# Optimization experiments

Measured on AMD Instinct MI355X. Metric: run time of the kernel, lower is better.

Reference implementation:

```python
import jax, jax.numpy as jnp
import numpy as np

B, D = 65536, 256      # batch, state dim (= hidden_dims[0])
H1, H2 = 256, 256      # hidden_dims
N_STEPS = 40           # fixed RK4 steps over t in [0, 1]
BN_EPS = 1e-3          # keras BatchNormalization default epsilon


def setup_inputs() -> dict:
    key = jax.random.key(0)
    ks = jax.random.split(key, 8)
    s = 0.05  # small init keeps dynamics smooth/stable
    return {
        "y0": jax.random.normal(ks[0], (B, D), dtype=jnp.float32),
        "W1": jax.random.normal(ks[1], (D, H1), dtype=jnp.float32) * s,
        "b1": jnp.zeros((H1,), jnp.float32),
        "g1": jnp.ones((H1,), jnp.float32),
        "be1": jnp.zeros((H1,), jnp.float32),
        "m1": jnp.zeros((H1,), jnp.float32),
        "v1": jnp.ones((H1,), jnp.float32),
        "W2": jax.random.normal(ks[2], (H1, H2), dtype=jnp.float32) * s,
        "b2": jnp.zeros((H2,), jnp.float32),
        "g2": jnp.ones((H2,), jnp.float32),
        "be2": jnp.zeros((H2,), jnp.float32),
        "m2": jnp.zeros((H2,), jnp.float32),
        "v2": jnp.ones((H2,), jnp.float32),
        "Wo": jax.random.normal(ks[3], (H2, D), dtype=jnp.float32) * s,
        "bo": jnp.zeros((D,), jnp.float32),
    }


def _ode_func(y, W1, b1, g1, be1, m1, v1, W2, b2, g2, be2, m2, v2, Wo, bo):
    # Dense(relu) -> BatchNorm(inference, moving stats) -> Dropout(inactive), x2, then Dense(tanh)
    h = jax.nn.relu(y @ W1 + b1)
    h = g1 * (h - m1) * jax.lax.rsqrt(v1 + BN_EPS) + be1
    h = jax.nn.relu(h @ W2 + b2)
    h = g2 * (h - m2) * jax.lax.rsqrt(v2 + BN_EPS) + be2
    return jnp.tanh(h @ Wo + bo)


def reference(y0, W1, b1, g1, be1, m1, v1, W2, b2, g2, be2, m2, v2, Wo, bo):
    # Integrate dy/dt = f(y) (autonomous) from t=0 to t=1 with fixed-step RK4.
    # (The original uses tfp adaptive BDF; RK4 is the clean deterministic stand-in
    # for the same continuous-time solution.)
    dt = jnp.float32(1.0 / N_STEPS)
    f = lambda y: _ode_func(y, W1, b1, g1, be1, m1, v1, W2, b2, g2, be2, m2, v2, Wo, bo)

    def step(y, _):
        k1 = f(y)
        k2 = f(y + 0.5 * dt * k1)
        k3 = f(y + 0.5 * dt * k2)
        k4 = f(y + dt * k3)
        return y + (dt / 6.0) * (k1 + 2.0 * k2 + 2.0 * k3 + k4), None

    y_final, _ = jax.lax.scan(step, y0, None, length=N_STEPS)
    return y_final
```

## Files before the change

### kernel.cpp

```cpp
#include <hip/hip_runtime.h>
#include <hip/hip_fp16.h>


typedef unsigned short u16;
typedef unsigned int   u32;
typedef __attribute__((ext_vector_type(8))) short bf16x8;
typedef __attribute__((ext_vector_type(4))) float f32x4;

#define BN_EPS 1e-3f
#define NROWS  65536
#define BM     128
#define NTHR   512
#define WT_ELEMS 196608
#define LDS_BIAS 131072
#define LDS_SIZE (131072 + 3072)

__device__ __forceinline__ u16 f2bf(float f) {
    u32 u = __float_as_uint(f);
    u32 r = u + 0x7FFFu + ((u >> 16) & 1u);
    return (u16)(r >> 16);
}
__device__ __forceinline__ float bf2f(u16 h) {
    return __uint_as_float(((u32)h) << 16);
}
__device__ __forceinline__ float fast_tanh(float x) {
    float e = __expf(2.0f * x);
    return 1.0f - __fdividef(2.0f, e + 1.0f);
}
__device__ __forceinline__ u32 pack_h2(float a, float b) {
    __half2 h = __floats2half2_rn(a, b);
    return *reinterpret_cast<u32*>(&h);
}
__device__ __forceinline__ float2 unpack_h2(u32 v) {
    __half2 h = *reinterpret_cast<__half2*>(&v);
    return __half22float2(h);
}
__device__ __forceinline__ u32 pack_bf2(float a, float b) {
    return ((u32)f2bf(b) << 16) | (u32)f2bf(a);
}
__device__ __forceinline__ float2 unpack_bf2(u32 p) {
    return make_float2(__uint_as_float(p << 16),
                       __uint_as_float(p & 0xFFFF0000u));
}

#define SWZ(row, kb) (((row) << 10) + ((kb) ^ (((row) & 7) << 4)))

__global__ void prep_bias(const float* __restrict__ b2,
                          const float* __restrict__ g1, const float* __restrict__ be1,
                          const float* __restrict__ m1, const float* __restrict__ v1,
                          const float* __restrict__ W2,
                          const float* __restrict__ bo,
                          const float* __restrict__ g2, const float* __restrict__ be2,
                          const float* __restrict__ m2, const float* __restrict__ v2,
                          const float* __restrict__ Wo,
                          float* __restrict__ b2o, float* __restrict__ boo) {
    int t = threadIdx.x;
    if (t < 256) {
        float s = b2[t];
        for (int i = 0; i < 256; ++i) {
            float s1 = g1[i] * rsqrtf(v1[i] + BN_EPS);
            float t1 = be1[i] - s1 * m1[i];
            s += t1 * W2[i * 256 + t];
        }
        b2o[t] = s;
    } else {
        int j = t - 256;
        float s = bo[j];
        for (int i = 0; i < 256; ++i) {
            float s2 = g2[i] * rsqrtf(v2[i] + BN_EPS);
            float t2 = be2[i] - s2 * m2[i];
            s += t2 * Wo[i * 256 + j];
        }
        boo[j] = s;
    }
}

__global__ void prep_weights(const float* __restrict__ W1, const float* __restrict__ W2,
                             const float* __restrict__ Wo,
                             const float* __restrict__ g1, const float* __restrict__ v1,
                             const float* __restrict__ g2, const float* __restrict__ v2,
                             u16* __restrict__ Wt) {
    int tid = blockIdx.x * 256 + threadIdx.x;
    if (tid >= 3 * 768 * 256) return;
    int l   = tid / (768 * 256);
    int r   = tid % (768 * 256);
    int kp  = r >> 8;
    int col = r & 255;
    int ok  = kp & 255;
    float w;
    if (l == 0)      w = W1[ok * 256 + col];
    else if (l == 1) w = W2[ok * 256 + col] * (g1[ok] * rsqrtf(v1[ok] + BN_EPS));
    else             w = Wo[ok * 256 + col] * (g2[ok] * rsqrtf(v2[ok] + BN_EPS));
    u16 hi = f2bf(w);
    u16 out = (kp < 512) ? hi : f2bf(w - bf2f(hi));
    int ks = kp >> 5, gg = (kp >> 3) & 3, j = kp & 7, cb = col >> 4, cc = col & 15;
    Wt[(size_t)l * WT_ELEMS + ks * 8192 + cb * 512 + cc * 32 + gg * 8 + j] = out;
}

__global__ __launch_bounds__(NTHR)
__attribute__((amdgpu_waves_per_eu(2, 2)))
void ode_persistent(const float* __restrict__ y0, float* __restrict__ yout,
                    const u16* __restrict__ Wt,
                    const float* __restrict__ b1, const float* __restrict__ b2o,
                    const float* __restrict__ boo) {
    extern __shared__ char smem[];
    float* bias_lds = reinterpret_cast<float*>(smem + LDS_BIAS);
    const int t = threadIdx.x;
    const size_t rowbase = (size_t)blockIdx.x * BM;
    const int lane = t & 63, wid = t >> 6;
    const int wr = wid >> 2, wc = wid & 3;
    const int c16 = lane & 15, g = lane >> 4;

    for (int i = t; i < 768; i += NTHR) {
        float v = (i < 256) ? b1[i] : ((i < 512) ? b2o[i - 256] : boo[i - 512]);
        bias_lds[i] = v;
    }

    f32x4 Y[4][4];
    u32   Kp[4][4][2];
    u32   A2[4][4][2];

#pragma unroll
    for (int m = 0; m < 4; ++m)
#pragma unroll
        for (int n = 0; n < 4; ++n) {
            const int col = wc * 64 + n * 16 + c16;
#pragma unroll
            for (int j = 0; j < 4; ++j) {
                const int row = wr * 64 + m * 16 + g * 4 + j;
                Y[m][n][j] = y0[(rowbase + row) * 256 + col];
            }
            Kp[m][n][0] = 0u; Kp[m][n][1] = 0u;
            A2[m][n][0] = 0u; A2[m][n][1] = 0u;
        }
    __syncthreads();

    const float dt  = 1.0f / 40.0f;
    const float c2  = 0.5f * dt;
    const float w16 = dt / 6.0f, w13 = dt / 3.0f;

    for (int it = 0; it < 160; ++it) {
        const int stage = it & 3;
        const float c = (stage == 0) ? 0.0f : ((stage == 3) ? dt : c2);
        const float w = (stage == 1 || stage == 2) ? w13 : w16;

#pragma unroll
        for (int m = 0; m < 4; ++m)
#pragma unroll
            for (int n = 0; n < 4; ++n) {
                const int col2 = (wc * 64 + n * 16 + c16) * 2;
                const float2 k01 = unpack_bf2(Kp[m][n][0]);
                const float2 k23 = unpack_bf2(Kp[m][n][1]);
                const float kj[4] = {k01.x, k01.y, k23.x, k23.y};
#pragma unroll
                for (int j = 0; j < 4; ++j) {
                    const int row = wr * 64 + m * 16 + g * 4 + j;
                    const float x = fmaf(c, kj[j], Y[m][n][j]);
                    const u32 xb = __float_as_uint(x);
                    const u16 hi = (u16)(xb >> 16);
                    const float fl = x - __uint_as_float(xb & 0xFFFF0000u);
                    *reinterpret_cast<u16*>(smem + SWZ(row, col2))       = hi;
                    *reinterpret_cast<u16*>(smem + SWZ(row, 512 + col2)) = f2bf(fl);
                }
            }
        __syncthreads();

        f32x4 ACC[4][4];

#pragma unroll 1
        for (int l = 0; l < 3; ++l) {
            const u16* __restrict__ wt = Wt + (size_t)l * WT_ELEMS;

#pragma unroll
            for (int n = 0; n < 4; ++n) {
                const float bv = bias_lds[l * 256 + wc * 64 + n * 16 + c16];
                const f32x4 b4 = {bv, bv, bv, bv};
#pragma unroll
                for (int m = 0; m < 4; ++m) ACC[m][n] = b4;
            }

#pragma unroll 2
            for (int ks = 0; ks < 24; ++ks) {
                const int kfull = ks * 32;
                const int kloc  = (kfull >= 512) ? (kfull - 512) : kfull;
                const int kb    = kloc * 2 + g * 16;
                bf16x8 av[4], bv[4];
#pragma unroll
                for (int m = 0; m < 4; ++m) {
                    const int row = wr * 64 + m * 16 + c16;
                    av[m] = *reinterpret_cast<const bf16x8*>(smem + SWZ(row, kb));
                }
                const u16* wp = wt + (size_t)(ks * 16 + wc * 4) * 512 + c16 * 32 + g * 8;
#pragma unroll
                for (int n = 0; n < 4; ++n)
                    bv[n] = *reinterpret_cast<const bf16x8*>(wp + n * 512);
#pragma unroll
                for (int m = 0; m < 4; ++m)
#pragma unroll
                    for (int n = 0; n < 4; ++n)
                        ACC[m][n] = __builtin_amdgcn_mfma_f32_16x16x32_bf16(
                            av[m], bv[n], ACC[m][n], 0, 0, 0);
            }
            __syncthreads();

            if (l < 2) {
#pragma unroll
                for (int m = 0; m < 4; ++m)
#pragma unroll
                    for (int n = 0; n < 4; ++n) {
                        const int col2 = (wc * 64 + n * 16 + c16) * 2;
#pragma unroll
                        for (int j = 0; j < 4; ++j) {
                            const int row = wr * 64 + m * 16 + g * 4 + j;
                            const float h = fmaxf(ACC[m][n][j], 0.0f);
                            const u32 hb = __float_as_uint(h);
                            const u16 hi = (u16)(hb >> 16);
                            const float fl = h - __uint_as_float(hb & 0xFFFF0000u);
                            *reinterpret_cast<u16*>(smem + SWZ(row, col2))       = hi;
                            *reinterpret_cast<u16*>(smem + SWZ(row, 512 + col2)) = f2bf(fl);
                        }
                    }
                __syncthreads();
            }
        }

        if (stage < 3) {
#pragma unroll
            for (int m = 0; m < 4; ++m)
#pragma unroll
                for (int n = 0; n < 4; ++n) {
                    const float t0 = fast_tanh(ACC[m][n][0]);
                    const float t1 = fast_tanh(ACC[m][n][1]);
                    const float t2 = fast_tanh(ACC[m][n][2]);
                    const float t3 = fast_tanh(ACC[m][n][3]);
                    Kp[m][n][0] = pack_bf2(t0, t1);
                    Kp[m][n][1] = pack_bf2(t2, t3);
                    const float2 p0 = unpack_h2(A2[m][n][0]);
                    const float2 p1 = unpack_h2(A2[m][n][1]);
                    A2[m][n][0] = pack_h2(fmaf(w, t0, p0.x), fmaf(w, t1, p0.y));
                    A2[m][n][1] = pack_h2(fmaf(w, t2, p1.x), fmaf(w, t3, p1.y));
                }
        } else {
#pragma unroll
            for (int m = 0; m < 4; ++m)
#pragma unroll
                for (int n = 0; n < 4; ++n) {
                    const float2 p0 = unpack_h2(A2[m][n][0]);
                    const float2 p1 = unpack_h2(A2[m][n][1]);
                    f32x4 yv = Y[m][n];
                    yv[0] += p0.x + w * fast_tanh(ACC[m][n][0]);
                    yv[1] += p0.y + w * fast_tanh(ACC[m][n][1]);
                    yv[2] += p1.x + w * fast_tanh(ACC[m][n][2]);
                    yv[3] += p1.y + w * fast_tanh(ACC[m][n][3]);
                    Y[m][n] = yv;
                    A2[m][n][0] = 0u; A2[m][n][1] = 0u;
                }
        }
    }

#pragma unroll
    for (int m = 0; m < 4; ++m)
#pragma unroll
        for (int n = 0; n < 4; ++n) {
            const int col = wc * 64 + n * 16 + c16;
#pragma unroll
            for (int j = 0; j < 4; ++j) {
                const int row = wr * 64 + m * 16 + g * 4 + j;
                yout[(rowbase + row) * 256 + col] = Y[m][n][j];
            }
        }
}

extern "C" void kernel_launch(void* const* d_in, const int* in_sizes, int n_in,
                              void* d_out, int out_size, void* d_ws, size_t ws_size,
                              hipStream_t stream) {
    const float* y0  = (const float*)d_in[0];
    const float* W1  = (const float*)d_in[1];
    const float* b1  = (const float*)d_in[2];
    const float* g1  = (const float*)d_in[3];
    const float* be1 = (const float*)d_in[4];
    const float* m1  = (const float*)d_in[5];
    const float* v1  = (const float*)d_in[6];
    const float* W2  = (const float*)d_in[7];
    const float* b2  = (const float*)d_in[8];
    const float* g2  = (const float*)d_in[9];
    const float* be2 = (const float*)d_in[10];
    const float* m2  = (const float*)d_in[11];
    const float* v2  = (const float*)d_in[12];
    const float* Wo  = (const float*)d_in[13];
    const float* bo  = (const float*)d_in[14];

    float* y = (float*)d_out;
    char*  ws = (char*)d_ws;
    const size_t MB = 1024 * 1024;
    u16*   Wt   = (u16*)(ws);
    float* b2o  = (float*)(ws + 2 * MB);
    float* boo  = b2o + 256;

    hipFuncSetAttribute(reinterpret_cast<const void*>(&ode_persistent),
                        hipFuncAttributeMaxDynamicSharedMemorySize, LDS_SIZE);

    prep_bias<<<1, 512, 0, stream>>>(b2, g1, be1, m1, v1, W2,
                                     bo, g2, be2, m2, v2, Wo, b2o, boo);
    prep_weights<<<2304, 256, 0, stream>>>(W1, W2, Wo, g1, v1, g2, v2, Wt);

    ode_persistent<<<NROWS / BM, NTHR, LDS_SIZE, stream>>>(y0, y, Wt, b1, b2o, boo);
}
```

Measured before the change: 17.78 ms.

## Drop lo×lo-weight split product and widen per-wave tiles to 128 rows

Replaces the 3-term bf16 split GEMM (a_hi·w_hi, a_lo·w_hi, a_hi·w_lo over K=768) with a structure where activations keep their hi/lo split but the weight lo correction is applied only against activation hi, which reorganizes K into 512 effective columns. The block drops to 256 threads (4 waves, each covering all 128 rows × 64 cols) with one wave per EU, so each weight fragment load is reused across 8 row tiles. The RK4 stage input (y + c·k) is now written to LDS directly in the epilogue, which removes the separate staging pass and the bf16-packed k registers. The risks are more register pressure with fewer waves to hide latency, and a change in numerical accuracy.

```diff
diff --git a/kernel.cpp b/kernel.cpp
--- a/kernel.cpp
+++ b/kernel.cpp
@@ -10,8 +10,8 @@
 #define BN_EPS 1e-3f
 #define NROWS  65536
 #define BM     128
-#define NTHR   512
-#define WT_ELEMS 196608
+#define NTHR   256
+#define WT_ELEMS 131072
 #define LDS_BIAS 131072
 #define LDS_SIZE (131072 + 3072)
 
@@ -35,15 +35,15 @@
     __half2 h = *reinterpret_cast<__half2*>(&v);
     return __half22float2(h);
 }
-__device__ __forceinline__ u32 pack_bf2(float a, float b) {
-    return ((u32)f2bf(b) << 16) | (u32)f2bf(a);
-}
-__device__ __forceinline__ float2 unpack_bf2(u32 p) {
-    return make_float2(__uint_as_float(p << 16),
-                       __uint_as_float(p & 0xFFFF0000u));
-}
 
 #define SWZ(row, kb) (((row) << 10) + ((kb) ^ (((row) & 7) << 4)))
+
+__device__ __forceinline__ void split_store(char* smem, int row, int col2, float x) {
+    const u32 xb = __float_as_uint(x);
+    *reinterpret_cast<u16*>(smem + SWZ(row, col2)) = (u16)(xb >> 16);
+    const float fl = x - __uint_as_float(xb & 0xFFFF0000u);
+    *reinterpret_cast<u16*>(smem + SWZ(row, 512 + col2)) = f2bf(fl);
+}
 
 __global__ void prep_bias(const float* __restrict__ b2,
                           const float* __restrict__ g1, const float* __restrict__ be1,
@@ -81,9 +81,9 @@
                              const float* __restrict__ g2, const float* __restrict__ v2,
                              u16* __restrict__ Wt) {
     int tid = blockIdx.x * 256 + threadIdx.x;
-    if (tid >= 3 * 768 * 256) return;
-    int l   = tid / (768 * 256);
-    int r   = tid % (768 * 256);
+    if (tid >= 3 * 512 * 256) return;
+    int l   = tid / (512 * 256);
+    int r   = tid % (512 * 256);
     int kp  = r >> 8;
     int col = r & 255;
     int ok  = kp & 255;
@@ -92,13 +92,13 @@
     else if (l == 1) w = W2[ok * 256 + col] * (g1[ok] * rsqrtf(v1[ok] + BN_EPS));
     else             w = Wo[ok * 256 + col] * (g2[ok] * rsqrtf(v2[ok] + BN_EPS));
     u16 hi = f2bf(w);
-    u16 out = (kp < 512) ? hi : f2bf(w - bf2f(hi));
+    u16 out = (kp < 256) ? hi : f2bf(w - bf2f(hi));
     int ks = kp >> 5, gg = (kp >> 3) & 3, j = kp & 7, cb = col >> 4, cc = col & 15;
     Wt[(size_t)l * WT_ELEMS + ks * 8192 + cb * 512 + cc * 32 + gg * 8 + j] = out;
 }
 
 __global__ __launch_bounds__(NTHR)
-__attribute__((amdgpu_waves_per_eu(2, 2)))
+__attribute__((amdgpu_waves_per_eu(1, 1)))
 void ode_persistent(const float* __restrict__ y0, float* __restrict__ yout,
                     const u16* __restrict__ Wt,
                     const float* __restrict__ b1, const float* __restrict__ b2o,
@@ -107,30 +107,30 @@
     float* bias_lds = reinterpret_cast<float*>(smem + LDS_BIAS);
     const int t = threadIdx.x;
     const size_t rowbase = (size_t)blockIdx.x * BM;
-    const int lane = t & 63, wid = t >> 6;
-    const int wr = wid >> 2, wc = wid & 3;
-    const int c16 = lane & 15, g = lane >> 4;
+    const int lane = t & 63;
+    const int wc   = t >> 6;
+    const int c16  = lane & 15, g = lane >> 4;
 
     for (int i = t; i < 768; i += NTHR) {
         float v = (i < 256) ? b1[i] : ((i < 512) ? b2o[i - 256] : boo[i - 512]);
         bias_lds[i] = v;
     }
 
-    f32x4 Y[4][4];
-    u32   Kp[4][4][2];
-    u32   A2[4][4][2];
-
-#pragma unroll
-    for (int m = 0; m < 4; ++m)
+    f32x4 Y [8][4];
+    u32   A2[8][4][2];
+
+#pragma unroll
+    for (int m = 0; m < 8; ++m)
 #pragma unroll
         for (int n = 0; n < 4; ++n) {
             const int col = wc * 64 + n * 16 + c16;
 #pragma unroll
             for (int j = 0; j < 4; ++j) {
-                const int row = wr * 64 + m * 16 + g * 4 + j;
-                Y[m][n][j] = y0[(rowbase + row) * 256 + col];
-            }
-            Kp[m][n][0] = 0u; Kp[m][n][1] = 0u;
+                const int row = m * 16 + g * 4 + j;
+                const float v = y0[(rowbase + row) * 256 + col];
+                Y[m][n][j] = v;
+                split_store(smem, row, col * 2, v);
+            }
             A2[m][n][0] = 0u; A2[m][n][1] = 0u;
         }
     __syncthreads();
@@ -139,33 +139,10 @@
     const float c2  = 0.5f * dt;
     const float w16 = dt / 6.0f, w13 = dt / 3.0f;
 
+#pragma unroll 1
     for (int it = 0; it < 160; ++it) {
-        const int stage = it & 3;
-        const float c = (stage == 0) ? 0.0f : ((stage == 3) ? dt : c2);
-        const float w = (stage == 1 || stage == 2) ? w13 : w16;
-
-#pragma unroll
-        for (int m = 0; m < 4; ++m)
-#pragma unroll
-            for (int n = 0; n < 4; ++n) {
-                const int col2 = (wc * 64 + n * 16 + c16) * 2;
-                const float2 k01 = unpack_bf2(Kp[m][n][0]);
-                const float2 k23 = unpack_bf2(Kp[m][n][1]);
-                const float kj[4] = {k01.x, k01.y, k23.x, k23.y};
-#pragma unroll
-                for (int j = 0; j < 4; ++j) {
-                    const int row = wr * 64 + m * 16 + g * 4 + j;
-                    const float x = fmaf(c, kj[j], Y[m][n][j]);
-                    const u32 xb = __float_as_uint(x);
-                    const u16 hi = (u16)(xb >> 16);
-                    const float fl = x - __uint_as_float(xb & 0xFFFF0000u);
-                    *reinterpret_cast<u16*>(smem + SWZ(row, col2))       = hi;
-                    *reinterpret_cast<u16*>(smem + SWZ(row, 512 + col2)) = f2bf(fl);
-                }
-            }
-        __syncthreads();
-
-        f32x4 ACC[4][4];
+        const int st = it & 3;
+        f32x4 ACC[8][4];
 
 #pragma unroll 1
         for (int l = 0; l < 3; ++l) {
@@ -176,96 +153,123 @@
                 const float bv = bias_lds[l * 256 + wc * 64 + n * 16 + c16];
                 const f32x4 b4 = {bv, bv, bv, bv};
 #pragma unroll
-                for (int m = 0; m < 4; ++m) ACC[m][n] = b4;
-            }
-
-#pragma unroll 2
-            for (int ks = 0; ks < 24; ++ks) {
-                const int kfull = ks * 32;
-                const int kloc  = (kfull >= 512) ? (kfull - 512) : kfull;
-                const int kb    = kloc * 2 + g * 16;
-                bf16x8 av[4], bv[4];
-#pragma unroll
-                for (int m = 0; m < 4; ++m) {
-                    const int row = wr * 64 + m * 16 + c16;
-                    av[m] = *reinterpret_cast<const bf16x8*>(smem + SWZ(row, kb));
-                }
+                for (int m = 0; m < 8; ++m) ACC[m][n] = b4;
+            }
+
+#pragma unroll 1
+            for (int ks = 0; ks < 8; ++ks) {
                 const u16* wp = wt + (size_t)(ks * 16 + wc * 4) * 512 + c16 * 32 + g * 8;
+                bf16x8 bv[4];
 #pragma unroll
                 for (int n = 0; n < 4; ++n)
                     bv[n] = *reinterpret_cast<const bf16x8*>(wp + n * 512);
-#pragma unroll
-                for (int m = 0; m < 4; ++m)
+                const int kb = ks * 64 + g * 16;
+#pragma unroll
+                for (int m = 0; m < 8; ++m) {
+                    const int row = m * 16 + c16;
+                    const bf16x8 ah = *reinterpret_cast<const bf16x8*>(smem + SWZ(row, kb));
+                    const bf16x8 al = *reinterpret_cast<const bf16x8*>(smem + SWZ(row, 512 + kb));
 #pragma unroll
                     for (int n = 0; n < 4; ++n)
                         ACC[m][n] = __builtin_amdgcn_mfma_f32_16x16x32_bf16(
-                            av[m], bv[n], ACC[m][n], 0, 0, 0);
+                            ah, bv[n], ACC[m][n], 0, 0, 0);
+#pragma unroll
+                    for (int n = 0; n < 4; ++n)
+                        ACC[m][n] = __builtin_amdgcn_mfma_f32_16x16x32_bf16(
+                            al, bv[n], ACC[m][n], 0, 0, 0);
+                }
+            }
+#pragma unroll 1
+            for (int ks = 8; ks < 16; ++ks) {
+                const u16* wp = wt + (size_t)(ks * 16 + wc * 4) * 512 + c16 * 32 + g * 8;
+                bf16x8 bv[4];
+#pragma unroll
+                for (int n = 0; n < 4; ++n)
+                    bv[n] = *reinterpret_cast<const bf16x8*>(wp + n * 512);
+                const int kb = (ks - 8) * 64 + g * 16;
+#pragma unroll
+                for (int m = 0; m < 8; ++m) {
+                    const int row = m * 16 + c16;
+                    const bf16x8 ah = *reinterpret_cast<const bf16x8*>(smem + SWZ(row, kb));
+#pragma unroll
+                    for (int n = 0; n < 4; ++n)
+                        ACC[m][n] = __builtin_amdgcn_mfma_f32_16x16x32_bf16(
+                            ah, bv[n], ACC[m][n], 0, 0, 0);
+                }
             }
             __syncthreads();
 
             if (l < 2) {
 #pragma unroll
-                for (int m = 0; m < 4; ++m)
+                for (int m = 0; m < 8; ++m)
 #pragma unroll
                     for (int n = 0; n < 4; ++n) {
                         const int col2 = (wc * 64 + n * 16 + c16) * 2;
 #pragma unroll
                         for (int j = 0; j < 4; ++j) {
-                            const int row = wr * 64 + m * 16 + g * 4 + j;
-                            const float h = fmaxf(ACC[m][n][j], 0.0f);
-                            const u32 hb = __float_as_uint(h);
-                            const u16 hi = (u16)(hb >> 16);
-                            const float fl = h - __uint_as_float(hb & 0xFFFF0000u);
-                            *reinterpret_cast<u16*>(smem + SWZ(row, col2))       = hi;
-                            *reinterpret_cast<u16*>(smem + SWZ(row, 512 + col2)) = f2bf(fl);
+                            const int row = m * 16 + g * 4 + j;
+                            split_store(smem, row, col2, fmaxf(ACC[m][n][j], 0.0f));
                         }
                     }
                 __syncthreads();
             }
         }
 
-        if (stage < 3) {
-#pragma unroll
-            for (int m = 0; m < 4; ++m)
+        if (st < 3) {
+            const float cn = (st == 2) ? dt : c2;
+            const float wa = (st == 0) ? w16 : w13;
+#pragma unroll
+            for (int m = 0; m < 8; ++m)
 #pragma unroll
                 for (int n = 0; n < 4; ++n) {
+                    const int col2 = (wc * 64 + n * 16 + c16) * 2;
                     const float t0 = fast_tanh(ACC[m][n][0]);
                     const float t1 = fast_tanh(ACC[m][n][1]);
                     const float t2 = fast_tanh(ACC[m][n][2]);
                     const float t3 = fast_tanh(ACC[m][n][3]);
-                    Kp[m][n][0] = pack_bf2(t0, t1);
-                    Kp[m][n][1] = pack_bf2(t2, t3);
                     const float2 p0 = unpack_h2(A2[m][n][0]);
                     const float2 p1 = unpack_h2(A2[m][n][1]);
-                    A2[m][n][0] = pack_h2(fmaf(w, t0, p0.x), fmaf(w, t1, p0.y));
-                    A2[m][n][1] = pack_h2(fmaf(w, t2, p1.x), fmaf(w, t3, p1.y));
+                    A2[m][n][0] = pack_h2(fmaf(wa, t0, p0.x), fmaf(wa, t1, p0.y));
+                    A2[m][n][1] = pack_h2(fmaf(wa, t2, p1.x), fmaf(wa, t3, p1.y));
+                    const int r0 = m * 16 + g * 4;
+                    split_store(smem, r0 + 0, col2, fmaf(cn, t0, Y[m][n][0]));
+                    split_store(smem, r0 + 1, col2, fmaf(cn, t1, Y[m][n][1]));
+                    split_store(smem, r0 + 2, col2, fmaf(cn, t2, Y[m][n][2]));
+                    split_store(smem, r0 + 3, col2, fmaf(cn, t3, Y[m][n][3]));
                 }
         } else {
 #pragma unroll
-            for (int m = 0; m < 4; ++m)
+            for (int m = 0; m < 8; ++m)
 #pragma unroll
                 for (int n = 0; n < 4; ++n) {
+                    const int col2 = (wc * 64 + n * 16 + c16) * 2;
                     const float2 p0 = unpack_h2(A2[m][n][0]);
                     const float2 p1 = unpack_h2(A2[m][n][1]);
                     f32x4 yv = Y[m][n];
-                    yv[0] += p0.x + w * fast_tanh(ACC[m][n][0]);
-                    yv[1] += p0.y + w * fast_tanh(ACC[m][n][1]);
-                    yv[2] += p1.x + w * fast_tanh(ACC[m][n][2]);
-                    yv[3] += p1.y + w * fast_tanh(ACC[m][n][3]);
+                    yv[0] += p0.x + w16 * fast_tanh(ACC[m][n][0]);
+                    yv[1] += p0.y + w16 * fast_tanh(ACC[m][n][1]);
+                    yv[2] += p1.x + w16 * fast_tanh(ACC[m][n][2]);
+                    yv[3] += p1.y + w16 * fast_tanh(ACC[m][n][3]);
                     Y[m][n] = yv;
+                    const int r0 = m * 16 + g * 4;
+                    split_store(smem, r0 + 0, col2, yv[0]);
+                    split_store(smem, r0 + 1, col2, yv[1]);
+                    split_store(smem, r0 + 2, col2, yv[2]);
+                    split_store(smem, r0 + 3, col2, yv[3]);
                     A2[m][n][0] = 0u; A2[m][n][1] = 0u;
                 }
         }
+        __syncthreads();
     }
 
 #pragma unroll
-    for (int m = 0; m < 4; ++m)
+    for (int m = 0; m < 8; ++m)
 #pragma unroll
         for (int n = 0; n < 4; ++n) {
             const int col = wc * 64 + n * 16 + c16;
 #pragma unroll
             for (int j = 0; j < 4; ++j) {
-                const int row = wr * 64 + m * 16 + g * 4 + j;
+                const int row = m * 16 + g * 4 + j;
                 yout[(rowbase + row) * 256 + col] = Y[m][n][j];
             }
         }
@@ -294,7 +298,7 @@
     char*  ws = (char*)d_ws;
     const size_t MB = 1024 * 1024;
     u16*   Wt   = (u16*)(ws);
-    float* b2o  = (float*)(ws + 2 * MB);
+    float* b2o  = (float*)(ws + 1 * MB);
     float* boo  = b2o + 256;
 
     hipFuncSetAttribute(reinterpret_cast<const void*>(&ode_persistent),
@@ -302,7 +306,7 @@
 
     prep_bias<<<1, 512, 0, stream>>>(b2, g1, be1, m1, v1, W2,
                                      bo, g2, be2, m2, v2, Wo, b2o, boo);
-    prep_weights<<<2304, 256, 0, stream>>>(W1, W2, Wo, g1, v1, g2, v2, Wt);
+    prep_weights<<<1536, 256, 0, stream>>>(W1, W2, Wo, g1, v1, g2, v2, Wt);
 
     ode_persistent<<<NROWS / BM, NTHR, LDS_SIZE, stream>>>(y0, y, Wt, b1, b2o, boo);
 }
```

Measured after the change: 30.50 ms. +71.6%, slower.
